# Kernel tuning notes

Measured on AMD Instinct MI355X. Metric: run time of the kernel, lower is better.

The kernel has to match this reference:

```python
import jax, jax.numpy as jnp
import numpy as np

IN_CH, OUT_CH, K, STRIDE = 128, 256, 3, 1

def setup_inputs() -> dict:
    key = jax.random.key(0)
    kx, kw = jax.random.split(key)
    x = jax.random.normal(kx, (32, IN_CH, 56, 56), dtype=jnp.float32)
    # xavier_uniform: bound = sqrt(6 / (fan_in + fan_out)), fans include receptive field
    fan_in = IN_CH * K * K
    fan_out = OUT_CH * K * K
    bound = float(np.sqrt(6.0 / (fan_in + fan_out)))
    weight = jax.random.uniform(kw, (OUT_CH, IN_CH, K, K), dtype=jnp.float32,
                                minval=-bound, maxval=bound)
    bias = jnp.zeros((OUT_CH,), dtype=jnp.float32)
    return {"x": x, "weight": weight, "bias": bias}

def reference(x, weight, bias):
    # VALID (no-padding) conv, stride STRIDE, NCHW layout, OIHW kernel
    out = jax.lax.conv_general_dilated(
        x, weight,
        window_strides=(STRIDE, STRIDE),
        padding="VALID",
        dimension_numbers=("NCHW", "OIHW", "NCHW"))
    return out + bias[None, :, None, None]
```

## Files before the change

kernel.cpp:

```cpp
#include <hip/hip_runtime.h>
#include <hip/hip_bf16.h>
#include <stdint.h>

#define NB    32
#define CIN   128
#define HIN   56
#define HW    (HIN*HIN)
#define OCH   256
#define OHW   54
#define SPB   (OHW*OHW)
#define KSZ   (CIN*9)
#define BM    128
#define BK    64
#define NKS   (KSZ/BK)
#define SPT   23

typedef __attribute__((ext_vector_type(8))) short bf16x8;
typedef __attribute__((ext_vector_type(4))) float f32x4;

typedef __attribute__((address_space(1))) const uint32_t g_u32;
typedef __attribute__((address_space(3))) uint32_t l_u32;
static __device__ __forceinline__ void gl_lds16(const void* g, void* l) {
    __builtin_amdgcn_global_load_lds((g_u32*)g, (l_u32*)l, 16, 0, 0);
}

__global__ void xpose_cast(const float* __restrict__ x, __hip_bfloat16* __restrict__ xt) {
    __shared__ float tile[32][33];
    const int hw0 = blockIdx.x * 32;
    const int c0  = blockIdx.y * 32;
    const int n   = blockIdx.z;
    const int tx = threadIdx.x, ty = threadIdx.y;
    const float* xp = x + ((size_t)n*CIN + c0)*HW + hw0;
    #pragma unroll
    for (int i = ty; i < 32; i += 8)
        tile[i][tx] = xp[(size_t)i*HW + tx];
    __syncthreads();
    const int t = ty*32 + tx;
    const int hwl = t >> 3, q = t & 7;
    ushort4 v;
    v.x = __bfloat16_as_ushort(__float2bfloat16(tile[q*4+0][hwl]));
    v.y = __bfloat16_as_ushort(__float2bfloat16(tile[q*4+1][hwl]));
    v.z = __bfloat16_as_ushort(__float2bfloat16(tile[q*4+2][hwl]));
    v.w = __bfloat16_as_ushort(__float2bfloat16(tile[q*4+3][hwl]));
    __hip_bfloat16* op = xt + ((size_t)n*HW + hw0 + hwl)*CIN + c0 + q*4;
    *(ushort4*)op = v;
}

__global__ void wcast(const float* __restrict__ w, __hip_bfloat16* __restrict__ wt) {
    int tid = blockIdx.x*256 + threadIdx.x;
    if (tid >= OCH*KSZ) return;
    int oc = tid / KSZ, r = tid % KSZ;
    int pos = r >> 7, ic = r & 127;
    wt[tid] = __float2bfloat16(w[((size_t)(oc*CIN + ic))*9 + pos]);
}

__global__ __launch_bounds__(256, 2)
void conv_mfma(const __hip_bfloat16* __restrict__ xt,
               const __hip_bfloat16* __restrict__ wt,
               const float* __restrict__ bias,
               float* __restrict__ out) {
    __shared__ char smem[64*132*4 >= 32768 ? 64*132*4 : 32768];
    uint4* Alds = (uint4*)smem;
    uint4* Blds = Alds + 1024;
    float (*eps)[132] = (float (*)[132])smem;

    const int t = threadIdx.x;
    const int sptile = blockIdx.x, octile = blockIdx.y, n = blockIdx.z;
    const int lane = t & 63, wid = t >> 6;
    const int wm = wid >> 1, wn = wid & 1;
    const int lr = lane & 15, lq = lane >> 4;

    const __hip_bfloat16* asrc[4];
    const __hip_bfloat16* bsrc[4];
    #pragma unroll
    for (int i = 0; i < 4; ++i) {
        int p = wid*256 + i*64 + lane;
        int row = p >> 3;
        int g = (p & 7) ^ (row & 7);
        asrc[i] = wt + (size_t)(octile*BM + row)*KSZ + g*8;
        int sp = sptile*BM + row; if (sp >= SPB) sp = SPB - 1;
        int oh = sp / OHW, ow = sp - oh*OHW;
        bsrc[i] = xt + ((size_t)(n*HIN + oh)*HIN + ow)*CIN + g*8;
    }

    auto issue = [&](int ks) {
        const int pos = ks >> 1;
        const int kh = pos / 3, kw = pos - kh*3;
        const int boff = (kh*HIN + kw)*CIN + (ks & 1)*64;
        const int aoff = ks*BK;
        #pragma unroll
        for (int i = 0; i < 4; ++i) {
            gl_lds16(asrc[i] + aoff, Alds + wid*256 + i*64);
            gl_lds16(bsrc[i] + boff, Blds + wid*256 + i*64);
        }
    };

    f32x4 acc[4][4];
    #pragma unroll
    for (int i = 0; i < 4; ++i)
        #pragma unroll
        for (int j = 0; j < 4; ++j)
            acc[i][j] = (f32x4){0.f, 0.f, 0.f, 0.f};

    issue(0);
    for (int ks = 0; ks < NKS; ++ks) {
        __syncthreads();
        bf16x8 a[2][4], b[2][4];
        #pragma unroll
        for (int kk = 0; kk < 2; ++kk)
            #pragma unroll
            for (int mi = 0; mi < 4; ++mi) {
                int ra = wm*64 + mi*16 + lr;
                a[kk][mi] = *(bf16x8*)&Alds[ra*8 + ((kk*4 + lq) ^ (ra & 7))];
                int rb = wn*64 + mi*16 + lr;
                b[kk][mi] = *(bf16x8*)&Blds[rb*8 + ((kk*4 + lq) ^ (rb & 7))];
            }
        __syncthreads();
        if (ks + 1 < NKS) issue(ks + 1);
        #pragma unroll
        for (int kk = 0; kk < 2; ++kk)
            #pragma unroll
            for (int mi = 0; mi < 4; ++mi)
                #pragma unroll
                for (int ni = 0; ni < 4; ++ni)
                    acc[mi][ni] = __builtin_amdgcn_mfma_f32_16x16x32_bf16(
                        a[kk][mi], b[kk][ni], acc[mi][ni], 0, 0, 0);
    }

    for (int h = 0; h < 2; ++h) {
        if (wm == h) {
            #pragma unroll
            for (int mi = 0; mi < 4; ++mi) {
                int rl = mi*16 + lq*4;
                #pragma unroll
                for (int ni = 0; ni < 4; ++ni) {
                    int cl = wn*64 + ni*16 + lr;
                    #pragma unroll
                    for (int r = 0; r < 4; ++r)
                        eps[rl + r][cl] = acc[mi][ni][r];
                }
            }
        }
        __syncthreads();
        const int cl4 = (t & 31) * 4;
        const int colg = sptile*BM + cl4;
        const int rsub = t >> 5;
        if (colg < SPB) {
            #pragma unroll
            for (int pass = 0; pass < 8; ++pass) {
                int rl = pass*8 + rsub;
                int rg = octile*BM + h*64 + rl;
                f32x4 v = *(f32x4*)&eps[rl][cl4];
                float bv = bias[rg];
                v = v + bv;
                *(f32x4*)&out[((size_t)n*OCH + rg)*SPB + colg] = v;
            }
        }
        __syncthreads();
    }
}

__global__ void conv_naive(const float* __restrict__ x, const float* __restrict__ w,
                           const float* __restrict__ bias, float* __restrict__ out) {
    size_t tid = (size_t)blockIdx.x*256 + threadIdx.x;
    const size_t total = (size_t)NB*OCH*SPB;
    if (tid >= total) return;
    int col = (int)(tid % SPB);
    int oc  = (int)((tid / SPB) % OCH);
    int n   = (int)(tid / ((size_t)SPB*OCH));
    int oh = col / OHW, ow = col % OHW;
    float s = bias[oc];
    for (int ic = 0; ic < CIN; ++ic)
        #pragma unroll
        for (int kh = 0; kh < 3; ++kh)
            #pragma unroll
            for (int kw = 0; kw < 3; ++kw)
                s += x[((size_t)(n*CIN+ic)*HIN + oh+kh)*HIN + ow+kw]
                   * w[((size_t)(oc*CIN+ic)*3 + kh)*3 + kw];
    out[tid] = s;
}

extern "C" void kernel_launch(void* const* d_in, const int* in_sizes, int n_in,
                              void* d_out, int out_size, void* d_ws, size_t ws_size,
                              hipStream_t stream) {
    const float* x    = (const float*)d_in[0];
    const float* w    = (const float*)d_in[1];
    const float* bias = (const float*)d_in[2];
    float* out = (float*)d_out;

    const size_t xt_bytes = (size_t)NB*HW*CIN*sizeof(__hip_bfloat16);
    const size_t wt_bytes = (size_t)OCH*KSZ*sizeof(__hip_bfloat16);

    if (ws_size >= xt_bytes + wt_bytes) {
        __hip_bfloat16* xt  = (__hip_bfloat16*)d_ws;
        __hip_bfloat16* wtp = (__hip_bfloat16*)((char*)d_ws + xt_bytes);
        hipLaunchKernelGGL(xpose_cast, dim3(HW/32, CIN/32, NB), dim3(32, 8), 0, stream, x, xt);
        hipLaunchKernelGGL(wcast, dim3((OCH*KSZ + 255)/256), dim3(256), 0, stream, w, wtp);
        hipLaunchKernelGGL(conv_mfma, dim3(SPT, OCH/BM, NB), dim3(256), 0, stream,
                           xt, wtp, bias, out);
    } else {
        size_t total = (size_t)NB*OCH*SPB;
        hipLaunchKernelGGL(conv_naive, dim3((unsigned)((total + 255)/256)), dim3(256), 0, stream,
                           x, w, bias, out);
    }
}
```

Baseline: 86.48 us.

## Enlarge conv GEMM tile to 128x256, flatten batch, and triple-buffer LDS loads

The implicit-GEMM conv kernel moves to 512-thread blocks covering 128 output channels by 256 spatial columns. The batch is folded into the column dimension, so tiles no longer waste work on a padded per-image remainder. Global-to-LDS loads become a three-stage ring buffer using explicit vmcnt waits. Next-stage loads are split across the two k-halves and interleaved with MFMA work, which runs at raised wave priority. The aim is to raise data reuse per block and hide load latency, at the cost of much more LDS per block and therefore lower occupancy.

```diff
diff --git a/kernel.cpp b/kernel.cpp
--- a/kernel.cpp
+++ b/kernel.cpp
@@ -11,9 +11,11 @@
 #define SPB   (OHW*OHW)
 #define KSZ   (CIN*9)
 #define BM    128
+#define BN    256
 #define BK    64
 #define NKS   (KSZ/BK)
-#define SPT   23
+#define TOTC  (NB*SPB)
+#define NT    365
 
 typedef __attribute__((ext_vector_type(8))) short bf16x8;
 typedef __attribute__((ext_vector_type(4))) float f32x4;
@@ -54,44 +56,52 @@
     wt[tid] = __float2bfloat16(w[((size_t)(oc*CIN + ic))*9 + pos]);
 }
 
-__global__ __launch_bounds__(256, 2)
+__global__ __launch_bounds__(512, 2)
 void conv_mfma(const __hip_bfloat16* __restrict__ xt,
                const __hip_bfloat16* __restrict__ wt,
                const float* __restrict__ bias,
                float* __restrict__ out) {
-    __shared__ char smem[64*132*4 >= 32768 ? 64*132*4 : 32768];
-    uint4* Alds = (uint4*)smem;
-    uint4* Blds = Alds + 1024;
-    float (*eps)[132] = (float (*)[132])smem;
+    __shared__ uint4 smem[3*3072];
 
     const int t = threadIdx.x;
-    const int sptile = blockIdx.x, octile = blockIdx.y, n = blockIdx.z;
+    const int tile = blockIdx.x, octile = blockIdx.y;
     const int lane = t & 63, wid = t >> 6;
-    const int wm = wid >> 1, wn = wid & 1;
+    const int wm = wid >> 2, wn = wid & 3;
     const int lr = lane & 15, lq = lane >> 4;
 
-    const __hip_bfloat16* asrc[4];
+    const __hip_bfloat16* asrc[2];
+    #pragma unroll
+    for (int i = 0; i < 2; ++i) {
+        int p = i*512 + t;
+        int row = p >> 3, g = (p & 7) ^ (row & 7);
+        asrc[i] = wt + (size_t)(octile*BM + row)*KSZ + g*8;
+    }
     const __hip_bfloat16* bsrc[4];
     #pragma unroll
     for (int i = 0; i < 4; ++i) {
-        int p = wid*256 + i*64 + lane;
-        int row = p >> 3;
-        int g = (p & 7) ^ (row & 7);
-        asrc[i] = wt + (size_t)(octile*BM + row)*KSZ + g*8;
-        int sp = sptile*BM + row; if (sp >= SPB) sp = SPB - 1;
-        int oh = sp / OHW, ow = sp - oh*OHW;
+        int p = i*512 + t;
+        int row = p >> 3, g = (p & 7) ^ (row & 7);
+        int colg = tile*BN + row; if (colg >= TOTC) colg = TOTC - 1;
+        int n = colg / SPB, rem = colg - n*SPB;
+        int oh = rem / OHW, ow = rem - oh*OHW;
         bsrc[i] = xt + ((size_t)(n*HIN + oh)*HIN + ow)*CIN + g*8;
     }
 
-    auto issue = [&](int ks) {
+    auto issue = [&](int ks, int part) {
+        uint4* Ab = smem + (ks % 3)*3072;
+        uint4* Bb = Ab + 1024;
         const int pos = ks >> 1;
         const int kh = pos / 3, kw = pos - kh*3;
+        const int aoff = ks*BK;
         const int boff = (kh*HIN + kw)*CIN + (ks & 1)*64;
-        const int aoff = ks*BK;
-        #pragma unroll
-        for (int i = 0; i < 4; ++i) {
-            gl_lds16(asrc[i] + aoff, Alds + wid*256 + i*64);
-            gl_lds16(bsrc[i] + boff, Blds + wid*256 + i*64);
+        if (part == 0) {
+            gl_lds16(asrc[0] + aoff, Ab + t);
+            gl_lds16(asrc[1] + aoff, Ab + 512 + t);
+            gl_lds16(bsrc[0] + boff, Bb + t);
+        } else {
+            gl_lds16(bsrc[1] + boff, Bb + 512 + t);
+            gl_lds16(bsrc[2] + boff, Bb + 1024 + t);
+            gl_lds16(bsrc[3] + boff, Bb + 1536 + t);
         }
     };
 
@@ -102,31 +112,46 @@
         for (int j = 0; j < 4; ++j)
             acc[i][j] = (f32x4){0.f, 0.f, 0.f, 0.f};
 
-    issue(0);
+    issue(0, 0); issue(0, 1);
+    issue(1, 0); issue(1, 1);
+
     for (int ks = 0; ks < NKS; ++ks) {
-        __syncthreads();
-        bf16x8 a[2][4], b[2][4];
+        if (ks < NKS-1) asm volatile("s_waitcnt vmcnt(6)" ::: "memory");
+        else            asm volatile("s_waitcnt vmcnt(0)" ::: "memory");
+        __builtin_amdgcn_s_barrier();
+        __builtin_amdgcn_sched_barrier(0);
+
+        const uint4* Ab = smem + (ks % 3)*3072;
+        const uint4* Bb = Ab + 1024;
+
         #pragma unroll
-        for (int kk = 0; kk < 2; ++kk)
+        for (int kk = 0; kk < 2; ++kk) {
+            if (ks + 2 < NKS) issue(ks + 2, kk);
+            bf16x8 a[4], b[4];
             #pragma unroll
             for (int mi = 0; mi < 4; ++mi) {
                 int ra = wm*64 + mi*16 + lr;
-                a[kk][mi] = *(bf16x8*)&Alds[ra*8 + ((kk*4 + lq) ^ (ra & 7))];
-                int rb = wn*64 + mi*16 + lr;
-                b[kk][mi] = *(bf16x8*)&Blds[rb*8 + ((kk*4 + lq) ^ (rb & 7))];
-            }
-        __syncthreads();
-        if (ks + 1 < NKS) issue(ks + 1);
-        #pragma unroll
-        for (int kk = 0; kk < 2; ++kk)
+                a[mi] = *(bf16x8*)&Ab[ra*8 + ((kk*4 + lq) ^ (ra & 7))];
+            }
+            #pragma unroll
+            for (int ni = 0; ni < 4; ++ni) {
+                int rb = wn*64 + ni*16 + lr;
+                b[ni] = *(bf16x8*)&Bb[rb*8 + ((kk*4 + lq) ^ (rb & 7))];
+            }
+            __builtin_amdgcn_s_setprio(1);
             #pragma unroll
             for (int mi = 0; mi < 4; ++mi)
                 #pragma unroll
                 for (int ni = 0; ni < 4; ++ni)
                     acc[mi][ni] = __builtin_amdgcn_mfma_f32_16x16x32_bf16(
-                        a[kk][mi], b[kk][ni], acc[mi][ni], 0, 0, 0);
-    }
-
+                        a[mi], b[ni], acc[mi][ni], 0, 0, 0);
+            __builtin_amdgcn_s_setprio(0);
+        }
+    }
+
+    __syncthreads();
+
+    float (*eps)[264] = (float (*)[264])smem;
     for (int h = 0; h < 2; ++h) {
         if (wm == h) {
             #pragma unroll
@@ -142,18 +167,19 @@
             }
         }
         __syncthreads();
-        const int cl4 = (t & 31) * 4;
-        const int colg = sptile*BM + cl4;
-        const int rsub = t >> 5;
-        if (colg < SPB) {
+        const int cl4 = (t & 63) * 4;
+        const int rsub = t >> 6;
+        const int colg = tile*BN + cl4;
+        if (colg < TOTC) {
+            const int n = colg / SPB;
+            const int sp = colg - n*SPB;
             #pragma unroll
             for (int pass = 0; pass < 8; ++pass) {
                 int rl = pass*8 + rsub;
                 int rg = octile*BM + h*64 + rl;
                 f32x4 v = *(f32x4*)&eps[rl][cl4];
-                float bv = bias[rg];
-                v = v + bv;
-                *(f32x4*)&out[((size_t)n*OCH + rg)*SPB + colg] = v;
+                v = v + bias[rg];
+                *(f32x4*)&out[((size_t)n*OCH + rg)*SPB + sp] = v;
             }
         }
         __syncthreads();
@@ -196,7 +222,7 @@
         __hip_bfloat16* wtp = (__hip_bfloat16*)((char*)d_ws + xt_bytes);
         hipLaunchKernelGGL(xpose_cast, dim3(HW/32, CIN/32, NB), dim3(32, 8), 0, stream, x, xt);
         hipLaunchKernelGGL(wcast, dim3((OCH*KSZ + 255)/256), dim3(256), 0, stream, w, wtp);
-        hipLaunchKernelGGL(conv_mfma, dim3(SPT, OCH/BM, NB), dim3(256), 0, stream,
+        hipLaunchKernelGGL(conv_mfma, dim3(NT, OCH/BM), dim3(512), 0, stream,
                            xt, wtp, bias, out);
     } else {
         size_t total = (size_t)NB*OCH*SPB;
```

New measurement: 89.26 us. +3.2%, slower.
